# Optimization experiments

Hardware: AMD Instinct MI355X
Metric: run time of the kernel (lower is better)

The kernel has to match this reference:

```python
import jax, jax.numpy as jnp
import numpy as np
import math

B, S, E, H = 2, 2048, 1024, 16
D = E // H          # d_k = 64 = n_qubits_per_head
F = 1024            # ffn_dim; MUST equal E for the original mixing to broadcast
LN_EPS = 1e-5


def _layernorm(x, g, b):
    m = jnp.mean(x, axis=-1, keepdims=True)
    v = jnp.var(x, axis=-1, keepdims=True)
    return (x - m) / jnp.sqrt(v + LN_EPS) * g + b


def _circuit_expvals(x):
    # Closed form of the variational circuit: RY(x_i) on wire i, RZ(theta_i),
    # CNOT chain (i -> i+1), measure PauliZ on each wire.
    # RZ is diagonal (no effect on Z probs); CNOT chain makes bit_i the XOR of
    # bits 0..i, so <Z_i> = prod_{j<=i} cos(x_j).
    return jnp.cumprod(jnp.cos(x), axis=-1)


def setup_inputs() -> dict:
    key = jax.random.key(0)
    ks = jax.random.split(key, 18)
    sc = 0.02
    inp = {
        "x": jax.random.normal(ks[0], (B, S, E), jnp.float32),
        "mask": jnp.ones((B, S), jnp.int32),
        "wq": jax.random.normal(ks[1], (E, E), jnp.float32) * sc,
        "wk": jax.random.normal(ks[2], (E, E), jnp.float32) * sc,
        "wv": jax.random.normal(ks[3], (E, E), jnp.float32) * sc,
        "wo": jax.random.normal(ks[4], (E, E), jnp.float32) * sc,
        "attn_param": jax.random.normal(ks[5], (D,), jnp.float32),   # RZ angles (no effect on expvals)
        "attn_qw": jnp.float32(0.5),
        "w1": jax.random.normal(ks[6], (E, F), jnp.float32) * sc,
        "b1": jnp.zeros((F,), jnp.float32),
        "w2": jax.random.normal(ks[7], (F, E), jnp.float32) * sc,
        "b2": jnp.zeros((E,), jnp.float32),
        "ffn_param": jax.random.normal(ks[8], (E,), jnp.float32),    # RZ angles (no effect on expvals)
        "ffn_qw": jnp.float32(0.5),
        "ln1_g": jnp.ones((E,), jnp.float32),
        "ln1_b": jnp.zeros((E,), jnp.float32),
        "ln2_g": jnp.ones((E,), jnp.float32),
        "ln2_b": jnp.zeros((E,), jnp.float32),
    }
    return inp


def reference(x, mask, wq, wk, wv, wo, attn_param, attn_qw,
              w1, b1, w2, b2, ffn_param, ffn_qw,
              ln1_g, ln1_b, ln2_g, ln2_b):
    b, s, _ = x.shape
    # ---- quantum attention sublayer (dropout inactive / eval mode) ----
    q = (x @ wq).reshape(b, s, H, D).transpose(0, 2, 1, 3)  # [b,h,s,d]
    k = (x @ wk).reshape(b, s, H, D).transpose(0, 2, 1, 3)
    v = (x @ wv).reshape(b, s, H, D).transpose(0, 2, 1, 3)
    scores = jnp.einsum("bhqd,bhkd->bhqk", q, k) / math.sqrt(D)
    scores = jnp.where(mask[:, None, None, :] == 0, -jnp.inf, scores)
    attn = jax.nn.softmax(scores, axis=-1)
    classical = jnp.einsum("bhqk,bhkd->bhqd", attn, v)
    quantum = _circuit_expvals(q)                             # [b,h,s,d]
    wgt = jax.nn.sigmoid(attn_qw)
    out = wgt * quantum + (1.0 - wgt) * classical
    attn_out = out.transpose(0, 2, 1, 3).reshape(b, s, E) @ wo
    x1 = _layernorm(x + attn_out, ln1_g, ln1_b)
    # ---- quantum feed-forward sublayer ----
    classical2 = jax.nn.relu(x1 @ w1 + b1)                    # [b,s,F]
    quantum2 = _circuit_expvals(x1)                           # [b,s,E] (E==F)
    wgt2 = jax.nn.sigmoid(ffn_qw)
    h = wgt2 * quantum2 + (1.0 - wgt2) * classical2
    ffn_out = h @ w2 + b2
    return _layernorm(x1 + ffn_out, ln2_g, ln2_b)
```

## Files before the change

kernel.cpp:

```cpp
#include <hip/hip_runtime.h>
#include <hip/hip_bf16.h>
#include <cmath>
#include <cstdint>


typedef __bf16 bf16_t;
typedef __bf16 bf16x8 __attribute__((ext_vector_type(8)));
typedef float f32x4 __attribute__((ext_vector_type(4)));
typedef unsigned short u16x4 __attribute__((ext_vector_type(4)));

#define DEV_INLINE __device__ __forceinline__
#define MB 1048576

DEV_INLINE void gload16(const void* g, void* lds) {
  __builtin_amdgcn_global_load_lds(
      (const __attribute__((address_space(1))) unsigned int*)g,
      (__attribute__((address_space(3))) unsigned int*)lds, 16, 0, 0);
}

DEV_INLINE unsigned short bf16_bits(float f) {
  bf16_t b = (bf16_t)f;
  return __builtin_bit_cast(unsigned short, b);
}

__global__ __launch_bounds__(256) void prep_kernel(
    const float* __restrict__ x, const float* __restrict__ wq,
    const float* __restrict__ wk, const float* __restrict__ wv,
    const float* __restrict__ wo, const float* __restrict__ w1,
    const float* __restrict__ w2, bf16_t* __restrict__ xc,
    bf16_t* __restrict__ wqkvT, bf16_t* __restrict__ wT3) {
  __shared__ bf16_t t[32][33];
  const int bid = blockIdx.x;
  if (bid < 2048) {
    const size_t i0 = ((size_t)bid * 256 + threadIdx.x) * 8;
    bf16x8 v;
#pragma unroll
    for (int j = 0; j < 8; ++j) v[j] = (bf16_t)x[i0 + j];
    *(bf16x8*)(xc + i0) = v;
    return;
  }
  const int grp = (bid - 2048) / 3072;
  const int tcb = (bid - 2048) - grp * 3072;
  const int mi = tcb >> 10;
  const float* src;
  bf16_t* dst;
  if (grp == 0) {
    src = (mi == 0) ? wq : (mi == 1) ? wk : wv;
    dst = wqkvT;
  } else {
    src = (mi == 0) ? wo : (mi == 1) ? w1 : w2;
    dst = wT3;
  }
  const int rem = tcb & 1023;
  const int bx = (rem & 31) * 32, by = (rem >> 5) * 32;
  const int tx = threadIdx.x & 31, ty = threadIdx.x >> 5;
#pragma unroll
  for (int i = 0; i < 4; ++i)
    t[ty + i * 8][tx] = (bf16_t)src[(size_t)(by + ty + i * 8) * 1024 + bx + tx];
  __syncthreads();
#pragma unroll
  for (int i = 0; i < 4; ++i)
    dst[(size_t)(mi * 1024 + bx + ty + i * 8) * 1024 + by + tx] = t[tx][ty + i * 8];
}

__global__ __launch_bounds__(256) void qkvvt_kernel(
    const bf16_t* __restrict__ xc, const bf16_t* __restrict__ wqkvT,
    bf16_t* __restrict__ qb, bf16_t* __restrict__ kb,
    bf16_t* __restrict__ vTb) {
  constexpr int K = 1024, BK = 64;
  __shared__ __align__(16) bf16_t As[128 * BK];
  __shared__ __align__(16) bf16_t Bs[128 * BK];

  const int tid = threadIdx.x;
  const int w = tid >> 6, lane = tid & 63;
  const int quad = lane >> 4, tc = lane & 15;
  const int bid = blockIdx.x;
  const int isqk = (bid < 512);
  int m0, n0;
  const bf16_t *Ab, *Bb;
  if (isqk) {
    n0 = (bid & 15) * 128;
    m0 = (bid >> 4) * 128;
    Ab = xc + (size_t)m0 * K;
    Bb = wqkvT + (size_t)n0 * K;
  } else {
    const int t = bid - 512;
    n0 = (t & 31) * 128;
    m0 = (t >> 5) * 128;
    Ab = wqkvT + (size_t)(2 * 1024 * 1024) + (size_t)m0 * K;
    Bb = xc + (size_t)n0 * K;
  }
  const int wm = (w >> 1) * 64, wn = (w & 1) * 64;
  const int srow = lane >> 3, scol = (lane & 7) * 8;

  f32x4 acc[4][4] = {};

  for (int k0 = 0; k0 < K; k0 += BK) {
    __syncthreads();
#pragma unroll
    for (int it = 0; it < 4; ++it) {
      const int rbase = w * 32 + it * 8;
      gload16(Ab + (size_t)(rbase + srow) * K + k0 + scol, &As[rbase * BK]);
      gload16(Bb + (size_t)(rbase + srow) * K + k0 + scol, &Bs[rbase * BK]);
    }
    __syncthreads();
#pragma unroll
    for (int ks = 0; ks < 2; ++ks) {
      bf16x8 af[4], bfv[4];
#pragma unroll
      for (int i = 0; i < 4; ++i)
        af[i] = *(const bf16x8*)&As[(wm + i * 16 + tc) * BK + ks * 32 + quad * 8];
#pragma unroll
      for (int j = 0; j < 4; ++j)
        bfv[j] = *(const bf16x8*)&Bs[(wn + j * 16 + tc) * BK + ks * 32 + quad * 8];
#pragma unroll
      for (int i = 0; i < 4; ++i)
#pragma unroll
        for (int j = 0; j < 4; ++j)
          acc[i][j] = __builtin_amdgcn_mfma_f32_16x16x32_bf16(af[i], bfv[j],
                                                              acc[i][j], 0, 0, 0);
    }
  }

#pragma unroll
  for (int i = 0; i < 4; ++i) {
#pragma unroll
    for (int j = 0; j < 4; ++j) {
      const int row0 = m0 + wm + i * 16 + quad * 4;
      const int col = n0 + wn + j * 16 + tc;
      if (isqk) {
        const int part = col >> 10, e = col & 1023, hh = e >> 6, d = e & 63;
        bf16_t* dst = part ? kb : qb;
#pragma unroll
        for (int r = 0; r < 4; ++r) {
          const int row = row0 + r;
          const int b = row >> 11, s = row & 2047;
          dst[((size_t)(b * 16 + hh) * 2048 + s) * 64 + d] = (bf16_t)acc[i][j][r];
        }
      } else {
        const int b = col >> 11, s = col & 2047;
#pragma unroll
        for (int r = 0; r < 4; ++r) {
          vTb[((size_t)(b * 1024 + row0 + r)) * 2048 + s] = (bf16_t)acc[i][j][r];
        }
      }
    }
  }
}

enum { EPI_WO = 2, EPI_W1 = 3, EPI_W2 = 4 };

template <int EPI>
__global__ __launch_bounds__(256) void gemm_bt_kernel(
    const bf16_t* __restrict__ A, const bf16_t* __restrict__ Bt,
    void* __restrict__ o0, const float* __restrict__ auxf,
    const bf16_t* __restrict__ auxb, const float* __restrict__ bias,
    const float* __restrict__ scal) {
  constexpr int K = 1024, BK = 64;
  __shared__ __align__(16) bf16_t As[64 * BK];
  __shared__ __align__(16) bf16_t Bs[64 * BK];

  const int tid = threadIdx.x;
  const int w = tid >> 6, lane = tid & 63;
  const int quad = lane >> 4, tc = lane & 15;
  const int m0 = blockIdx.y * 64, n0 = blockIdx.x * 64;
  const int wm = (w >> 1) * 32, wn = (w & 1) * 32;
  const int srow = lane >> 3, scol = (lane & 7) * 8;

  f32x4 acc[2][2] = {};

  const bf16_t* Ab = A + (size_t)m0 * K;
  const bf16_t* Bb = Bt + (size_t)n0 * K;

  for (int k0 = 0; k0 < K; k0 += BK) {
    __syncthreads();
#pragma unroll
    for (int it = 0; it < 2; ++it) {
      const int rbase = w * 16 + it * 8;
      gload16(Ab + (size_t)(rbase + srow) * K + k0 + scol, &As[rbase * BK]);
      gload16(Bb + (size_t)(rbase + srow) * K + k0 + scol, &Bs[rbase * BK]);
    }
    __syncthreads();
#pragma unroll
    for (int ks = 0; ks < 2; ++ks) {
      bf16x8 af[2], bfv[2];
#pragma unroll
      for (int i = 0; i < 2; ++i)
        af[i] = *(const bf16x8*)&As[(wm + i * 16 + tc) * BK + ks * 32 + quad * 8];
#pragma unroll
      for (int j = 0; j < 2; ++j)
        bfv[j] = *(const bf16x8*)&Bs[(wn + j * 16 + tc) * BK + ks * 32 + quad * 8];
#pragma unroll
      for (int i = 0; i < 2; ++i)
#pragma unroll
        for (int j = 0; j < 2; ++j)
          acc[i][j] = __builtin_amdgcn_mfma_f32_16x16x32_bf16(af[i], bfv[j],
                                                              acc[i][j], 0, 0, 0);
    }
  }

  float wsig = 0.f;
  if (EPI == EPI_W1) wsig = 1.f / (1.f + __expf(-scal[0]));

#pragma unroll
  for (int i = 0; i < 2; ++i) {
#pragma unroll
    for (int j = 0; j < 2; ++j) {
      const int row0 = m0 + wm + i * 16 + quad * 4;
      const int col = n0 + wn + j * 16 + tc;
      if (EPI == EPI_WO) {
#pragma unroll
        for (int r = 0; r < 4; ++r) {
          const int row = row0 + r;
          ((float*)o0)[(size_t)row * 1024 + col] =
              acc[i][j][r] + auxf[(size_t)row * 1024 + col];
        }
      } else if (EPI == EPI_W1) {
#pragma unroll
        for (int r = 0; r < 4; ++r) {
          const int row = row0 + r;
          float c = fmaxf(acc[i][j][r] + bias[col], 0.f);
          const float qv = (float)auxb[(size_t)row * 1024 + col];
          ((bf16_t*)o0)[(size_t)row * 1024 + col] =
              (bf16_t)(wsig * qv + (1.f - wsig) * c);
        }
      } else {
#pragma unroll
        for (int r = 0; r < 4; ++r) {
          const int row = row0 + r;
          ((float*)o0)[(size_t)row * 1024 + col] =
              acc[i][j][r] + bias[col] + (float)auxb[(size_t)row * 1024 + col];
        }
      }
    }
  }
}

__global__ __launch_bounds__(256) void attn_kernel(
    const bf16_t* __restrict__ q, const bf16_t* __restrict__ k,
    const bf16_t* __restrict__ vT, const float* __restrict__ aqw,
    bf16_t* __restrict__ out) {
  constexpr int S = 2048, LDK = 72;
  __shared__ __align__(16) bf16_t Ks[64 * LDK];
  __shared__ __align__(16) bf16_t Vs[64 * LDK];
  __shared__ __align__(16) bf16_t Ps[4][32 * LDK];
  __shared__ bf16_t Ql[128 * LDK];
  __shared__ float segp[128][4];

  const int tid = threadIdx.x, w = tid >> 6, lane = tid & 63;
  const int quad = lane >> 4, tc = lane & 15;
  const int bh = blockIdx.y, q0 = blockIdx.x * 128;
  const bf16_t* qg = q + ((size_t)bh * S + q0) * 64;
  const bf16_t* kg = k + (size_t)bh * S * 64;
  const bf16_t* vg = vT + (size_t)bh * 64 * S;

  const int strow = tid >> 2, stcol = (tid & 3) * 16;

  bf16x8 pk0 = *(const bf16x8*)(kg + (size_t)strow * 64 + stcol);
  bf16x8 pk1 = *(const bf16x8*)(kg + (size_t)strow * 64 + stcol + 8);
  bf16x8 pv0 = *(const bf16x8*)(vg + (size_t)strow * S + stcol);
  bf16x8 pv1 = *(const bf16x8*)(vg + (size_t)strow * S + stcol + 8);

  {
    float c[2][16];
    const int ss = tid & 3;
#pragma unroll
    for (int pass = 0; pass < 2; ++pass) {
      const int rr = pass * 64 + (tid >> 2);
      const bf16_t* qr = qg + rr * 64 + ss * 16;
      float p = 1.f;
#pragma unroll
      for (int j2 = 0; j2 < 16; ++j2) {
        c[pass][j2] = __cosf((float)qr[j2]);
        p *= c[pass][j2];
      }
      segp[rr][ss] = p;
    }
    __syncthreads();
#pragma unroll
    for (int pass = 0; pass < 2; ++pass) {
      const int rr = pass * 64 + (tid >> 2);
      float pre = 1.f;
      for (int u = 0; u < ss; ++u) pre *= segp[rr][u];
#pragma unroll
      for (int j2 = 0; j2 < 16; ++j2) {
        pre *= c[pass][j2];
        Ql[rr * LDK + ss * 16 + j2] = (bf16_t)pre;
      }
    }
  }

  bf16x8 aq[2][2];
#pragma unroll
  for (int qs = 0; qs < 2; ++qs) {
    const int qrow = w * 32 + qs * 16 + tc;
#pragma unroll
    for (int ks = 0; ks < 2; ++ks) {
      bf16x8 t = *(const bf16x8*)(qg + qrow * 64 + ks * 32 + quad * 8);
#pragma unroll
      for (int e = 0; e < 8; ++e) t[e] = (bf16_t)((float)t[e] * 0.18033688f);
      aq[qs][ks] = t;
    }
  }

  float lacc[2] = {0.f, 0.f};
  f32x4 o[2][4] = {};
  bf16_t* Pw = Ps[w];

  for (int kt = 0; kt < S; kt += 64) {
    __syncthreads();
    *(bf16x8*)&Ks[strow * LDK + stcol] = pk0;
    *(bf16x8*)&Ks[strow * LDK + stcol + 8] = pk1;
    *(bf16x8*)&Vs[strow * LDK + stcol] = pv0;
    *(bf16x8*)&Vs[strow * LDK + stcol + 8] = pv1;
    if (kt + 64 < S) {
      const int nk = kt + 64;
      pk0 = *(const bf16x8*)(kg + (size_t)(nk + strow) * 64 + stcol);
      pk1 = *(const bf16x8*)(kg + (size_t)(nk + strow) * 64 + stcol + 8);
      pv0 = *(const bf16x8*)(vg + (size_t)strow * S + nk + stcol);
      pv1 = *(const bf16x8*)(vg + (size_t)strow * S + nk + stcol + 8);
    }
    __syncthreads();

    f32x4 sf[2][4] = {};
#pragma unroll
    for (int ks = 0; ks < 2; ++ks) {
#pragma unroll
      for (int nt = 0; nt < 4; ++nt) {
        bf16x8 ak = *(const bf16x8*)&Ks[(nt * 16 + tc) * LDK + ks * 32 + quad * 8];
        sf[0][nt] = __builtin_amdgcn_mfma_f32_16x16x32_bf16(ak, aq[0][ks], sf[0][nt], 0, 0, 0);
        sf[1][nt] = __builtin_amdgcn_mfma_f32_16x16x32_bf16(ak, aq[1][ks], sf[1][nt], 0, 0, 0);
      }
    }

#pragma unroll
    for (int qs = 0; qs < 2; ++qs) {
#pragma unroll
      for (int nt = 0; nt < 4; ++nt) {
        u16x4 pk;
        float ps = 0.f;
#pragma unroll
        for (int r = 0; r < 4; ++r) {
          const float p = __builtin_amdgcn_exp2f(sf[qs][nt][r]);
          ps += p;
          pk[r] = bf16_bits(p);
        }
        lacc[qs] += ps;
        *(u16x4*)&Pw[(qs * 16 + tc) * LDK + nt * 16 + quad * 4] = pk;
      }
    }
    asm volatile("s_waitcnt lgkmcnt(0)" ::: "memory");

#pragma unroll
    for (int ks = 0; ks < 2; ++ks) {
      bf16x8 ap0 = *(const bf16x8*)&Pw[tc * LDK + ks * 32 + quad * 8];
      bf16x8 ap1 = *(const bf16x8*)&Pw[(16 + tc) * LDK + ks * 32 + quad * 8];
#pragma unroll
      for (int j = 0; j < 4; ++j) {
        bf16x8 bv = *(const bf16x8*)&Vs[(j * 16 + tc) * LDK + ks * 32 + quad * 8];
        o[0][j] = __builtin_amdgcn_mfma_f32_16x16x32_bf16(ap0, bv, o[0][j], 0, 0, 0);
        o[1][j] = __builtin_amdgcn_mfma_f32_16x16x32_bf16(ap1, bv, o[1][j], 0, 0, 0);
      }
    }
  }

#pragma unroll
  for (int qs = 0; qs < 2; ++qs) {
    lacc[qs] += __shfl_xor(lacc[qs], 16, 64);
    lacc[qs] += __shfl_xor(lacc[qs], 32, 64);
  }

  const float wsig = 1.f / (1.f + __expf(-aqw[0]));
  const int b = bh >> 4, h = bh & 15;
#pragma unroll
  for (int qs = 0; qs < 2; ++qs) {
#pragma unroll
    for (int r = 0; r < 4; ++r) {
      const int lr = quad * 4 + r;
      const float linv = 1.f / __shfl(lacc[qs], lr, 64);
      const int lrow = w * 32 + qs * 16 + lr;
      const int sg = q0 + lrow;
#pragma unroll
      for (int j = 0; j < 4; ++j) {
        const int d = j * 16 + tc;
        const float cl = o[qs][j][r] * linv;
        const float qv = (float)Ql[lrow * LDK + d];
        out[((size_t)(b * 2048 + sg)) * 1024 + h * 64 + d] =
            (bf16_t)(wsig * qv + (1.f - wsig) * cl);
      }
    }
  }
}

__global__ __launch_bounds__(256) void ln1scan_kernel(
    const float* __restrict__ res, const float* __restrict__ g,
    const float* __restrict__ bta, bf16_t* __restrict__ x1,
    bf16_t* __restrict__ q2) {
  const int row = blockIdx.x;
  const int tid = threadIdx.x, w = tid >> 6, lane = tid & 63;
  f32x4 v = *(const f32x4*)&res[(size_t)row * 1024 + tid * 4];
  float s = v[0] + v[1] + v[2] + v[3];
  float sq = v[0] * v[0] + v[1] * v[1] + v[2] * v[2] + v[3] * v[3];
#pragma unroll
  for (int off = 32; off >= 1; off >>= 1) {
    s += __shfl_xor(s, off, 64);
    sq += __shfl_xor(sq, off, 64);
  }
  __shared__ float rs[4], rq[4], wtot[4];
  if (lane == 0) {
    rs[w] = s;
    rq[w] = sq;
  }
  __syncthreads();
  s = rs[0] + rs[1] + rs[2] + rs[3];
  sq = rq[0] + rq[1] + rq[2] + rq[3];
  const float mean = s * (1.f / 1024.f);
  const float var = fmaxf(sq * (1.f / 1024.f) - mean * mean, 0.f);
  const float rstd = rsqrtf(var + 1e-5f);

  const f32x4 gv = *(const f32x4*)&g[tid * 4];
  const f32x4 bv = *(const f32x4*)&bta[tid * 4];
  float c[4], p = 1.f;
  u16x4 xb;
#pragma unroll
  for (int i = 0; i < 4; ++i) {
    const float y = (v[i] - mean) * rstd * gv[i] + bv[i];
    const bf16_t yb = (bf16_t)y;
    xb[i] = __builtin_bit_cast(unsigned short, yb);
    c[i] = __cosf((float)yb);
    p *= c[i];
  }
  *(u16x4*)&x1[(size_t)row * 1024 + tid * 4] = xb;

  float ip = p;
#pragma unroll
  for (int off = 1; off < 64; off <<= 1) {
    const float t = __shfl_up(ip, off, 64);
    if (lane >= off) ip *= t;
  }
  if (lane == 63) wtot[w] = ip;
  __syncthreads();
  float carry = 1.f;
  for (int u = 0; u < w; ++u) carry *= wtot[u];
  float run = __shfl_up(ip, 1, 64);
  if (lane == 0) run = 1.f;
  run *= carry;
  u16x4 qv;
#pragma unroll
  for (int i = 0; i < 4; ++i) {
    run *= c[i];
    qv[i] = bf16_bits(run);
  }
  *(u16x4*)&q2[(size_t)row * 1024 + tid * 4] = qv;
}

__global__ __launch_bounds__(256) void ln2_kernel(
    const float* __restrict__ res, const float* __restrict__ g,
    const float* __restrict__ bta, float* __restrict__ out) {
  const int row = blockIdx.x;
  const int tid = threadIdx.x, w = tid >> 6, lane = tid & 63;
  f32x4 v = *(const f32x4*)&res[(size_t)row * 1024 + tid * 4];
  float s = v[0] + v[1] + v[2] + v[3];
  float sq = v[0] * v[0] + v[1] * v[1] + v[2] * v[2] + v[3] * v[3];
#pragma unroll
  for (int off = 32; off >= 1; off >>= 1) {
    s += __shfl_xor(s, off, 64);
    sq += __shfl_xor(sq, off, 64);
  }
  __shared__ float rs[4], rq[4];
  if (lane == 0) {
    rs[w] = s;
    rq[w] = sq;
  }
  __syncthreads();
  s = rs[0] + rs[1] + rs[2] + rs[3];
  sq = rq[0] + rq[1] + rq[2] + rq[3];
  const float mean = s * (1.f / 1024.f);
  const float var = fmaxf(sq * (1.f / 1024.f) - mean * mean, 0.f);
  const float rstd = rsqrtf(var + 1e-5f);
  const f32x4 gv = *(const f32x4*)&g[tid * 4];
  const f32x4 bv = *(const f32x4*)&bta[tid * 4];
  f32x4 y;
#pragma unroll
  for (int i = 0; i < 4; ++i) y[i] = (v[i] - mean) * rstd * gv[i] + bv[i];
  *(f32x4*)&out[(size_t)row * 1024 + tid * 4] = y;
}

extern "C" void kernel_launch(void* const* d_in, const int* in_sizes, int n_in,
                              void* d_out, int out_size, void* d_ws,
                              size_t ws_size, hipStream_t stream) {
  (void)in_sizes;
  (void)n_in;
  (void)out_size;
  (void)ws_size;
  const float* x = (const float*)d_in[0];
  const float* wq = (const float*)d_in[2];
  const float* wk = (const float*)d_in[3];
  const float* wv = (const float*)d_in[4];
  const float* wo = (const float*)d_in[5];
  const float* attn_qw = (const float*)d_in[7];
  const float* w1 = (const float*)d_in[8];
  const float* b1 = (const float*)d_in[9];
  const float* w2 = (const float*)d_in[10];
  const float* b2 = (const float*)d_in[11];
  const float* ffn_qw = (const float*)d_in[13];
  const float* ln1_g = (const float*)d_in[14];
  const float* ln1_b = (const float*)d_in[15];
  const float* ln2_g = (const float*)d_in[16];
  const float* ln2_b = (const float*)d_in[17];

  char* ws = (char*)d_ws;
  char* wsout = (char*)d_out;
  bf16_t* wT3 = (bf16_t*)(ws + 0);
  bf16_t* wqkvT = (bf16_t*)(ws + 6 * MB);
  bf16_t* xc = (bf16_t*)(ws + 12 * MB);
  bf16_t* qb = (bf16_t*)(ws + 20 * MB);
  bf16_t* aout = (bf16_t*)(ws + 6 * MB);
  float* res = (float*)(ws + 14 * MB);
  bf16_t* x1 = (bf16_t*)(ws + 6 * MB);
  float* res2 = (float*)(ws + 14 * MB);
  bf16_t* kb = (bf16_t*)(wsout + 0);
  bf16_t* vTb = (bf16_t*)(wsout + 8 * MB);
  bf16_t* q2 = (bf16_t*)(wsout + 0);
  bf16_t* hbuf = (bf16_t*)(wsout + 8 * MB);

  const dim3 tb(256);

  prep_kernel<<<8192, tb, 0, stream>>>(x, wq, wk, wv, wo, w1, w2, xc, wqkvT, wT3);

  qkvvt_kernel<<<768, tb, 0, stream>>>(xc, wqkvT, qb, kb, vTb);

  attn_kernel<<<dim3(16, 32), tb, 0, stream>>>(qb, kb, vTb, attn_qw, aout);

  gemm_bt_kernel<EPI_WO><<<dim3(16, 64), tb, 0, stream>>>(
      aout, wT3, res, x, nullptr, nullptr, nullptr);

  ln1scan_kernel<<<4096, tb, 0, stream>>>(res, ln1_g, ln1_b, x1, q2);

  gemm_bt_kernel<EPI_W1><<<dim3(16, 64), tb, 0, stream>>>(
      x1, wT3 + 1024 * 1024, hbuf, nullptr, q2, b1, ffn_qw);

  gemm_bt_kernel<EPI_W2><<<dim3(16, 64), tb, 0, stream>>>(
      hbuf, wT3 + 2 * 1024 * 1024, res2, nullptr, x1, b2, nullptr);

  ln2_kernel<<<4096, tb, 0, stream>>>(res2, ln2_g, ln2_b, (float*)d_out);
}
```

Baseline: 288.9 us.

## Rewrite QKV projection GEMM with 256x256 tiles, double-buffered async LDS, swizzle

Replaces the 128x128 QKV/V^T GEMM (768 blocks, 256 threads, single-buffered) with a 256x256-tile kernel using 512 threads and 192 blocks. Global-to-LDS loads are double-buffered so the next K-slab is fetched while MFMAs run on the current one, coordinated with raw barriers and explicit vmcnt/lgkmcnt waits. LDS addresses are XOR-swizzled to avoid bank conflicts, and s_setprio raises priority around MFMA bursts. The 128KB LDS footprint and larger accumulator register use limit occupancy, and 192 blocks may underfill the CUs on mi355x.

After: 273.7 us. 5.2% less time.

```diff
diff --git a/kernel.cpp b/kernel.cpp
--- a/kernel.cpp
+++ b/kernel.cpp
@@ -63,67 +63,115 @@
     dst[(size_t)(mi * 1024 + bx + ty + i * 8) * 1024 + by + tx] = t[tx][ty + i * 8];
 }
 
-__global__ __launch_bounds__(256) void qkvvt_kernel(
+DEV_INLINE void stage_tile(const char* __restrict__ G, char* ldsT, int k0b,
+                           int wid, int lane) {
+#pragma unroll
+  for (int t = 0; t < 4; ++t) {
+    const int plin = t * 8192 + wid * 1024 + lane * 16;
+    const int p = plin ^ ((((unsigned)plin >> 7) & 7) << 4);
+    gload16(G + (size_t)(p >> 7) * 2048 + k0b + (p & 127),
+            ldsT + t * 8192 + wid * 1024);
+  }
+}
+
+DEV_INLINE void compute_tile(const char* lds_tile, int wm, int wn, int quad,
+                             int tc, f32x4 (&acc)[8][4]) {
+  const char* Ab = lds_tile;
+  const char* Bb = lds_tile + 32768;
+#pragma unroll
+  for (int ks = 0; ks < 2; ++ks) {
+    const int colb = ks * 64 + quad * 16;
+    bf16x8 bfv[4];
+#pragma unroll
+    for (int j = 0; j < 4; ++j) {
+      const int r = wn + j * 16 + tc;
+      bfv[j] = *(const bf16x8*)(Bb + ((r * 128 + colb) ^ ((r & 7) << 4)));
+    }
+#pragma unroll
+    for (int ih = 0; ih < 2; ++ih) {
+      bf16x8 af[4];
+#pragma unroll
+      for (int i = 0; i < 4; ++i) {
+        const int r = wm + (ih * 4 + i) * 16 + tc;
+        af[i] = *(const bf16x8*)(Ab + ((r * 128 + colb) ^ ((r & 7) << 4)));
+      }
+      __builtin_amdgcn_s_setprio(1);
+#pragma unroll
+      for (int i = 0; i < 4; ++i)
+#pragma unroll
+        for (int j = 0; j < 4; ++j)
+          acc[ih * 4 + i][j] = __builtin_amdgcn_mfma_f32_16x16x32_bf16(
+              af[i], bfv[j], acc[ih * 4 + i][j], 0, 0, 0);
+      __builtin_amdgcn_s_setprio(0);
+    }
+  }
+}
+
+#define BAR_PRE_LGKM asm volatile("s_waitcnt lgkmcnt(0)" ::: "memory")
+#define BAR_PRE_VM8 asm volatile("s_waitcnt vmcnt(8)" ::: "memory")
+#define RAW_BAR                       \
+  __builtin_amdgcn_s_barrier();       \
+  asm volatile("" ::: "memory")
+
+__global__ __launch_bounds__(512, 2) void qkvvt8_kernel(
     const bf16_t* __restrict__ xc, const bf16_t* __restrict__ wqkvT,
     bf16_t* __restrict__ qb, bf16_t* __restrict__ kb,
     bf16_t* __restrict__ vTb) {
-  constexpr int K = 1024, BK = 64;
-  __shared__ __align__(16) bf16_t As[128 * BK];
-  __shared__ __align__(16) bf16_t Bs[128 * BK];
-
-  const int tid = threadIdx.x;
-  const int w = tid >> 6, lane = tid & 63;
+  __shared__ __align__(16) char lds[131072];
+  const int tid = threadIdx.x, wid = tid >> 6, lane = tid & 63;
   const int quad = lane >> 4, tc = lane & 15;
   const int bid = blockIdx.x;
-  const int isqk = (bid < 512);
+  const int isqk = (bid < 128);
   int m0, n0;
-  const bf16_t *Ab, *Bb;
+  const char *A, *B;
   if (isqk) {
-    n0 = (bid & 15) * 128;
-    m0 = (bid >> 4) * 128;
-    Ab = xc + (size_t)m0 * K;
-    Bb = wqkvT + (size_t)n0 * K;
+    m0 = (bid >> 3) * 256;
+    n0 = (bid & 7) * 256;
+    A = (const char*)(xc + (size_t)m0 * 1024);
+    B = (const char*)(wqkvT + (size_t)n0 * 1024);
   } else {
-    const int t = bid - 512;
-    n0 = (t & 31) * 128;
-    m0 = (t >> 5) * 128;
-    Ab = wqkvT + (size_t)(2 * 1024 * 1024) + (size_t)m0 * K;
-    Bb = xc + (size_t)n0 * K;
-  }
-  const int wm = (w >> 1) * 64, wn = (w & 1) * 64;
-  const int srow = lane >> 3, scol = (lane & 7) * 8;
-
-  f32x4 acc[4][4] = {};
-
-  for (int k0 = 0; k0 < K; k0 += BK) {
-    __syncthreads();
-#pragma unroll
-    for (int it = 0; it < 4; ++it) {
-      const int rbase = w * 32 + it * 8;
-      gload16(Ab + (size_t)(rbase + srow) * K + k0 + scol, &As[rbase * BK]);
-      gload16(Bb + (size_t)(rbase + srow) * K + k0 + scol, &Bs[rbase * BK]);
-    }
-    __syncthreads();
-#pragma unroll
-    for (int ks = 0; ks < 2; ++ks) {
-      bf16x8 af[4], bfv[4];
-#pragma unroll
-      for (int i = 0; i < 4; ++i)
-        af[i] = *(const bf16x8*)&As[(wm + i * 16 + tc) * BK + ks * 32 + quad * 8];
-#pragma unroll
-      for (int j = 0; j < 4; ++j)
-        bfv[j] = *(const bf16x8*)&Bs[(wn + j * 16 + tc) * BK + ks * 32 + quad * 8];
-#pragma unroll
-      for (int i = 0; i < 4; ++i)
-#pragma unroll
-        for (int j = 0; j < 4; ++j)
-          acc[i][j] = __builtin_amdgcn_mfma_f32_16x16x32_bf16(af[i], bfv[j],
-                                                              acc[i][j], 0, 0, 0);
-    }
-  }
-
-#pragma unroll
-  for (int i = 0; i < 4; ++i) {
+    const int t2 = bid - 128;
+    m0 = (t2 >> 4) * 256;
+    n0 = (t2 & 15) * 256;
+    A = (const char*)(wqkvT + (size_t)(2 * 1024 * 1024) + (size_t)m0 * 1024);
+    B = (const char*)(xc + (size_t)n0 * 1024);
+  }
+  const int wm = (wid >> 2) * 128, wn = (wid & 3) * 64;
+
+  f32x4 acc[8][4] = {};
+
+  stage_tile(A, lds, 0, wid, lane);
+  stage_tile(B, lds + 32768, 0, wid, lane);
+  stage_tile(A, lds + 65536, 128, wid, lane);
+  stage_tile(B, lds + 98304, 128, wid, lane);
+  BAR_PRE_VM8;
+  RAW_BAR;
+
+  for (int it = 0; it < 7; ++it) {
+    const int k0b = it * 256 + 256;
+    compute_tile(lds, wm, wn, quad, tc, acc);
+    BAR_PRE_LGKM;
+    RAW_BAR;
+    stage_tile(A, lds, k0b, wid, lane);
+    stage_tile(B, lds + 32768, k0b, wid, lane);
+    BAR_PRE_VM8;
+    RAW_BAR;
+    compute_tile(lds + 65536, wm, wn, quad, tc, acc);
+    BAR_PRE_LGKM;
+    RAW_BAR;
+    stage_tile(A, lds + 65536, k0b + 128, wid, lane);
+    stage_tile(B, lds + 98304, k0b + 128, wid, lane);
+    BAR_PRE_VM8;
+    RAW_BAR;
+  }
+  compute_tile(lds, wm, wn, quad, tc, acc);
+  asm volatile("s_waitcnt vmcnt(0)" ::: "memory");
+  BAR_PRE_LGKM;
+  RAW_BAR;
+  compute_tile(lds + 65536, wm, wn, quad, tc, acc);
+
+#pragma unroll
+  for (int i = 0; i < 8; ++i) {
 #pragma unroll
     for (int j = 0; j < 4; ++j) {
       const int row0 = m0 + wm + i * 16 + quad * 4;
@@ -528,7 +576,7 @@
 
   prep_kernel<<<8192, tb, 0, stream>>>(x, wq, wk, wv, wo, w1, w2, xc, wqkvT, wT3);
 
-  qkvvt_kernel<<<768, tb, 0, stream>>>(xc, wqkvT, qb, kb, vTb);
+  qkvvt8_kernel<<<192, dim3(512), 0, stream>>>(xc, wqkvT, qb, kb, vTb);
 
   attn_kernel<<<dim3(16, 32), tb, 0, stream>>>(qb, kb, vTb, attn_qw, aout);
 
```
